# Performance work log

Hardware: AMD Instinct MI355X
Metric: run time of the kernel (lower is better)

The kernel has to match this reference:

```python
import jax, jax.numpy as jnp
import numpy as np

B, L = 8, 16384
H = 64          # num_channel
N2 = 32         # s4_hidden_size // 2 complex conjugate-pair modes
DEPTH = 4       # model_depth
NLAYERS = 1 + DEPTH  # number of DSSM layers
EPS = 1e-5


def setup_inputs() -> dict:
    key = jax.random.key(0)
    ks = jax.random.split(key, 12)
    x = jax.random.normal(ks[0], (B, L), dtype=jnp.float32)
    # input linear 1 -> H
    w_in = jax.random.normal(ks[1], (H,), dtype=jnp.float32)
    b_in = jax.random.normal(ks[2], (H,), dtype=jnp.float32) * 0.1
    # hidden linears H -> H
    w_mid = jax.random.normal(ks[3], (DEPTH, H, H), dtype=jnp.float32) / np.sqrt(H)
    b_mid = jax.random.normal(ks[4], (DEPTH, H), dtype=jnp.float32) * 0.1
    # output linear H -> 1
    w_out = jax.random.normal(ks[5], (H,), dtype=jnp.float32) / np.sqrt(H)
    b_out = jax.random.normal(ks[6], (), dtype=jnp.float32) * 0.1
    # S4D / DSSM parameters (stacked over the 5 SSM layers)
    log_dt = (jax.random.uniform(ks[7], (NLAYERS, H), dtype=jnp.float32)
              * (np.log(0.1) - np.log(0.001)) + np.log(0.001))
    log_A_real = jnp.log(0.5 * jnp.ones((NLAYERS, H, N2), dtype=jnp.float32))
    A_imag = jnp.pi * jnp.broadcast_to(jnp.arange(N2, dtype=jnp.float32), (NLAYERS, H, N2))
    C_re = jax.random.normal(ks[8], (NLAYERS, H, N2), dtype=jnp.float32)
    C_im = jax.random.normal(ks[9], (NLAYERS, H, N2), dtype=jnp.float32)
    D = jax.random.normal(ks[10], (NLAYERS, H), dtype=jnp.float32)
    return {"x": x, "w_in": w_in, "b_in": b_in, "w_mid": w_mid, "b_mid": b_mid,
            "w_out": w_out, "b_out": b_out, "log_dt": log_dt,
            "log_A_real": log_A_real, "A_imag": A_imag,
            "C_re": C_re, "C_im": C_im, "D": D}


def _dssm(u, log_dt, log_A_real, A_imag, C_re, C_im, D):
    # u: [B, H, L]; diagonal SSM applied as FFT convolution (S4D ZOH kernel)
    Lq = u.shape[-1]
    dt = jnp.exp(log_dt)                      # [H]
    A = -jnp.exp(log_A_real) + 1j * A_imag    # [H, N2]
    dtA = A * dt[:, None]                     # [H, N2]
    C_eff = (C_re + 1j * C_im) * (jnp.exp(dtA) - 1.0) / A
    # Vandermonde: exp(dtA * l) for l in [0, L)
    V = jnp.exp(dtA[:, :, None] * jnp.arange(Lq, dtype=jnp.float32))  # [H, N2, L]
    k = 2.0 * jnp.einsum('hn,hnl->hl', C_eff, V).real                # [H, L]
    uf = jnp.fft.rfft(u, n=2 * Lq)
    kf = jnp.fft.rfft(k, n=2 * Lq)
    y = jnp.fft.irfft(uf * kf, n=2 * Lq)[..., :Lq]
    return y + u * D[:, None]


def reference(x, w_in, b_in, w_mid, b_mid, w_out, b_out,
              log_dt, log_A_real, A_imag, C_re, C_im, D):
    # side chain: Abs -> Decibel -> Linear(1,H) -> tanh -> [DSSM -> tanh] ...
    s = 20.0 * jnp.log10(jnp.abs(x) + EPS)            # [B, L]
    h = jnp.tanh(s[..., None] * w_in + b_in)          # [B, L, H]
    h = jnp.tanh(_dssm(h.transpose(0, 2, 1), log_dt[0], log_A_real[0],
                       A_imag[0], C_re[0], C_im[0], D[0]).transpose(0, 2, 1))
    for i in range(DEPTH):
        h = jnp.tanh(jnp.einsum('blh,oh->blo', h, w_mid[i]) + b_mid[i])
        j = i + 1
        h = jnp.tanh(_dssm(h.transpose(0, 2, 1), log_dt[j], log_A_real[j],
                           A_imag[j], C_re[j], C_im[j], D[j]).transpose(0, 2, 1))
    g = jnp.einsum('blh,h->bl', h, w_out) + b_out      # [B, L]
    g = jnp.power(10.0, g / 20.0)                      # Amplitude (dB -> linear)
    return x * g
```

## Files before the change

### kernel.cpp

```cpp
#include <hip/hip_runtime.h>
#include <math.h>

#define Bq 8
#define Lq 16384
#define Hq 64
#define N2q 32
#define NLAYERSq 5

typedef _Float16 f16x8 __attribute__((ext_vector_type(8)));
typedef _Float16 f16x4 __attribute__((ext_vector_type(4)));
typedef _Float16 f16x2 __attribute__((ext_vector_type(2)));
typedef float    f32x4 __attribute__((ext_vector_type(4)));

#define MFMA16F(a, b, c) __builtin_amdgcn_mfma_f32_16x16x32_f16(a, b, c, 0, 0, 0)

#define UT_OFF    0
#define SS_OFF    32768
#define SMEM_SZ   50176
#define YST_OFF   0

#define WT_OFF_B   0
#define WP_OFF_B   163840
#define A2_OFF_B   (163840 + 5242880)
#define W16_OFF_B  (163840 + 5242880 + 15728640)
#define U_OFF_B    (163840 + 5242880 + 15728640 + 32768)

__device__ __forceinline__ float fast_tanh(float y) {
    float e = __expf(2.0f * y);
    return 1.0f - 2.0f * __builtin_amdgcn_rcpf(e + 1.0f);
}

__global__ __launch_bounds__(256)
void k_prep(const float* __restrict__ log_dt, const float* __restrict__ log_A_real,
            const float* __restrict__ A_imag, const float* __restrict__ C_re,
            const float* __restrict__ C_im, const float* __restrict__ Dvec,
            const float* __restrict__ w_mid,
            float* __restrict__ wT_tab, _Float16* __restrict__ Wp,
            _Float16* __restrict__ A2, _Float16* __restrict__ W16) {
    __shared__ float Pr[129][33], Pi[129][33];
    __shared__ float cre[32], cim[32], Kv[128];
    __shared__ double sdAr[32], sdAi[32];
    const int ph = blockIdx.x >> 2;
    const int qt = blockIdx.x & 3;
    const int tid = threadIdx.x;

    if (qt == 0 && ph < 256 && tid < 64) {
        int e = ph * 64 + tid;
        W16[e] = (_Float16)w_mid[e];
    }

    if (tid < 32) {
        int n = tid;
        int pidx = ph * N2q + n;
        double dt  = exp((double)log_dt[ph]);
        double aRe = -exp((double)log_A_real[pidx]);
        double aIm = (double)A_imag[pidx];
        double dAr = aRe * dt, dAi = aIm * dt;
        sdAr[n] = dAr; sdAi[n] = dAi;
        double er  = exp(dAr);
        double wre = er * cos(dAi), wim = er * sin(dAi);
        double Er = wre - 1.0, Ei = wim;
        double inv = 1.0 / (aRe * aRe + aIm * aIm);
        double Fr = (Er * aRe + Ei * aIm) * inv;
        double Fi = (Ei * aRe - Er * aIm) * inv;
        double Cr = (double)C_re[pidx], Ci = (double)C_im[pidx];
        cre[n] = (float)(2.0 * (Cr * Fr - Ci * Fi));
        cim[n] = (float)(2.0 * (Cr * Fi + Ci * Fr));
        if (qt == 0) {
            double qr = wre, qi = wim;
            #pragma unroll
            for (int s = 0; s < 7; s++) {
                double nr = qr * qr - qi * qi;
                qi = 2.0 * qr * qi; qr = nr;
            }
            float wTr = (float)qr, wTi = (float)qi;
            #pragma unroll
            for (int s = 0; s < 4; s++) {
                double nr = qr * qr - qi * qi;
                qi = 2.0 * qr * qi; qr = nr;
            }
            float* wt = wT_tab + ph * 128 + n * 4;
            wt[0] = wTr; wt[1] = wTi; wt[2] = (float)qr; wt[3] = (float)qi;
        }
    }
    __syncthreads();

    const double TWO_PI  = 6.2831853071795864769;
    const double INV_2PI = 0.15915494309189533577;
    for (int e = tid; e < 129 * 32; e += 256) {
        int j = e >> 5, n = e & 31;
        double phd = (double)j * sdAi[n];
        double r   = fma(-TWO_PI, nearbyint(phd * INV_2PI), phd);
        float  mag = __expf((float)((double)j * sdAr[n]));
        float  rf  = (float)r;
        Pr[j][n] = mag * cosf(rf);
        Pi[j][n] = mag * sinf(rf);
    }
    __syncthreads();

    if (tid < 128) {
        int d = tid;
        float s = 0.f;
        #pragma unroll 8
        for (int n = 0; n < 32; n++)
            s += cre[n] * Pr[d][n] - cim[n] * Pi[d][n];
        if (d == 0) s += Dvec[ph];
        Kv[d] = s;
    }
    __syncthreads();

    {
        _Float16* wpb = Wp + (size_t)ph * 8192;
        int o = tid;
        int kk = (qt << 4) + (o >> 4);
        int l0 = (o & 15) * 8;
        f16x8 v;
        #pragma unroll
        for (int j = 0; j < 8; j++) {
            int l = l0 + j;
            v[j] = (_Float16)((kk < 32) ? Pr[127 - l][kk] : Pi[127 - l][kk - 32]);
        }
        *(f16x8*)(wpb + kk * 128 + l0) = v;
    }
    {
        _Float16* a2b = A2 + (size_t)ph * 24576;
        for (int o = tid; o < 768; o += 256) {
            int m  = (qt << 5) + (o / 24);
            int k0 = (o % 24) * 8;
            f16x8 v;
            #pragma unroll
            for (int j = 0; j < 8; j++) {
                int k = k0 + j;
                float f;
                if (k < 128) {
                    f = (k <= m) ? Kv[m - k] : 0.f;
                } else {
                    int kk = k - 128, n2 = kk & 31;
                    float pr = Pr[m + 1][n2], pi2 = Pi[m + 1][n2];
                    f = (kk < 32) ? (cre[n2] * pr - cim[n2] * pi2)
                                  : -(cre[n2] * pi2 + cim[n2] * pr);
                }
                v[j] = (_Float16)f;
            }
            *(f16x8*)(a2b + m * 192 + k0) = v;
        }
    }
}

__global__ __launch_bounds__(256, 3)
void k_scan(const float* __restrict__ x, _Float16* __restrict__ u16,
            const _Float16* __restrict__ Wp_all, const _Float16* __restrict__ A2_all,
            const float* __restrict__ wT_all, int layer,
            const float* __restrict__ w_in, const float* __restrict__ b_in) {
    extern __shared__ char smem[];
    char* UT = smem + UT_OFF;
    char* Sf = smem + SS_OFF;
    char* St = smem + SS_OFF;
    char* yst = smem + YST_OFF;

    const int bh = blockIdx.x;
    const int h  = bh & 63;
    const int tid = threadIdx.x;
    const int lane = tid & 63;
    const int wave = tid >> 6;
    const int ph = layer * 64 + h;
    const _Float16* Wp = Wp_all + (size_t)ph * 8192;
    const _Float16* A2 = A2_all + (size_t)ph * 24576;
    const float* wT4 = wT_all + ph * 128;
    _Float16* uu = u16 + ((size_t)bh << 14);

    const int rA = lane & 15;
    const int qA = lane >> 4;

    if (layer == 0) {
        const float* xb = x + ((size_t)(bh >> 6) << 14);
        const float wi = w_in[h], bi = b_in[h];
        for (int it = 0; it < 8; ++it) {
            int flat8 = (it * 256 + tid) * 8;
            int n = flat8 >> 7, k = flat8 & 127;
            float4 a = *(const float4*)(xb + flat8);
            float4 b = *(const float4*)(xb + flat8 + 4);
            float f[8] = {a.x, a.y, a.z, a.w, b.x, b.y, b.z, b.w};
            f16x8 hv;
            #pragma unroll
            for (int j = 0; j < 8; j++) {
                float s = 6.0205999132796239f * __log2f(fabsf(f[j]) + 1e-5f);
                hv[j] = (_Float16)fast_tanh(fmaf(s, wi, bi));
            }
            *(f16x8*)(UT + n * 256 + ((k * 2) ^ ((n & 7) << 4))) = hv;
        }
    } else {
        for (int it = 0; it < 8; ++it) {
            int flat8 = (it * 256 + tid) * 8;
            int n = flat8 >> 7, k = flat8 & 127;
            f16x8 hv = *(const f16x8*)(uu + flat8);
            *(f16x8*)(UT + n * 256 + ((k * 2) ^ ((n & 7) << 4))) = hv;
        }
    }
    __syncthreads();

    {
        f32x4 acc1[8];
        #pragma unroll
        for (int nt = 0; nt < 8; nt++) acc1[nt] = (f32x4){0.f, 0.f, 0.f, 0.f};
        for (int ks = 0; ks < 4; ks++) {
            f16x8 af = *(const f16x8*)(Wp + (wave * 16 + rA) * 128 + ks * 32 + qA * 8);
            #pragma unroll
            for (int nt = 0; nt < 8; nt++) {
                int n = nt * 16 + rA;
                f16x8 bv = *(const f16x8*)(UT + n * 256 + ((ks * 64 + qA * 16) ^ ((n & 7) << 4)));
                acc1[nt] = MFMA16F(af, bv, acc1[nt]);
            }
        }
        #pragma unroll
        for (int nt = 0; nt < 8; nt++) {
            int c = nt * 16 + rA;
            #pragma unroll
            for (int r = 0; r < 4; r++)
                *(_Float16*)(Sf + (wave * 16 + qA * 4 + r) * 272 + c * 2) = (_Float16)acc1[nt][r];
        }
    }
    __syncthreads();

    {
        const int sn = tid >> 3;
        const int ss = tid & 7;
        const float wTr = wT4[sn * 4 + 0], wTi = wT4[sn * 4 + 1];
        float fr[16], fi[16];
        {
            f16x8 a0 = *(const f16x8*)(Sf + sn * 272 + ss * 32);
            f16x8 a1 = *(const f16x8*)(Sf + sn * 272 + ss * 32 + 16);
            f16x8 b0 = *(const f16x8*)(Sf + (sn + 32) * 272 + ss * 32);
            f16x8 b1 = *(const f16x8*)(Sf + (sn + 32) * 272 + ss * 32 + 16);
            #pragma unroll
            for (int j = 0; j < 8; j++) {
                fr[j] = (float)a0[j]; fr[j + 8] = (float)a1[j];
                fi[j] = (float)b0[j]; fi[j + 8] = (float)b1[j];
            }
        }
        float Tr = 0.f, Ti = 0.f;
        #pragma unroll
        for (int i = 0; i < 16; i++) {
            float nTr = fmaf(wTr, Tr, fmaf(-wTi, Ti, fr[i]));
            Ti = fmaf(wTr, Ti, fmaf(wTi, Tr, fi[i]));
            Tr = nTr;
        }
        float gr = wT4[sn * 4 + 2], gi = wT4[sn * 4 + 3];
        #pragma unroll
        for (int s = 0; s < 3; s++) {
            float pr = __shfl_up(Tr, 1 << s, 8);
            float pi = __shfl_up(Ti, 1 << s, 8);
            if (ss >= (1 << s)) {
                Tr = fmaf(gr, pr, fmaf(-gi, pi, Tr));
                Ti = fmaf(gr, pi, fmaf(gi, pr, Ti));
            }
            float ngr = fmaf(gr, gr, -gi * gi);
            gi = 2.f * gr * gi; gr = ngr;
        }
        float Er_ = __shfl_up(Tr, 1, 8);
        float Ei_ = __shfl_up(Ti, 1, 8);
        if (ss == 0) { Er_ = 0.f; Ei_ = 0.f; }
        __syncthreads();
        float Gr = Er_, Gi = Ei_;
        #pragma unroll
        for (int i = 0; i < 16; i++) {
            int c = ss * 16 + i;
            int sw = (c & 7) << 4;
            *(_Float16*)(St + c * 128 + ((sn * 2) ^ sw))        = (_Float16)Gr;
            *(_Float16*)(St + c * 128 + (((sn + 32) * 2) ^ sw)) = (_Float16)Gi;
            float nGr = fmaf(wTr, Gr, fmaf(-wTi, Gi, fr[i]));
            Gi = fmaf(wTr, Gi, fmaf(wTi, Gr, fi[i]));
            Gr = nGr;
        }
    }
    __syncthreads();

    f32x4 acc[2][8];
    #pragma unroll
    for (int mi = 0; mi < 2; mi++)
        #pragma unroll
        for (int nt = 0; nt < 8; nt++) acc[mi][nt] = (f32x4){0.f, 0.f, 0.f, 0.f};
    #pragma unroll
    for (int mi = 0; mi < 2; mi++) {
        const _Float16* Arow = A2 + ((wave * 2 + mi) * 16 + rA) * 192;
        for (int ks = 0; ks < 4; ks++) {
            f16x8 af = *(const f16x8*)(Arow + ks * 32 + qA * 8);
            #pragma unroll
            for (int nt = 0; nt < 8; nt++) {
                int n = nt * 16 + rA;
                f16x8 bv = *(const f16x8*)(UT + n * 256 + ((ks * 64 + qA * 16) ^ ((n & 7) << 4)));
                acc[mi][nt] = MFMA16F(af, bv, acc[mi][nt]);
            }
        }
        #pragma unroll
        for (int ks2 = 0; ks2 < 2; ks2++) {
            f16x8 af = *(const f16x8*)(Arow + 128 + ks2 * 32 + qA * 8);
            #pragma unroll
            for (int nt = 0; nt < 8; nt++) {
                int c = nt * 16 + rA;
                f16x8 bv = *(const f16x8*)(St + c * 128 + ((ks2 * 64 + qA * 16) ^ ((c & 7) << 4)));
                acc[mi][nt] = MFMA16F(af, bv, acc[mi][nt]);
            }
        }
    }
    __syncthreads();

    #pragma unroll
    for (int mi = 0; mi < 2; mi++) {
        int m0 = (wave * 2 + mi) * 16 + qA * 4;
        #pragma unroll
        for (int nt = 0; nt < 8; nt++) {
            int c = nt * 16 + rA;
            f16x4 o;
            o[0] = (_Float16)fast_tanh(acc[mi][nt][0]);
            o[1] = (_Float16)fast_tanh(acc[mi][nt][1]);
            o[2] = (_Float16)fast_tanh(acc[mi][nt][2]);
            o[3] = (_Float16)fast_tanh(acc[mi][nt][3]);
            *(f16x4*)(yst + c * 272 + m0 * 2) = o;
        }
    }
    __syncthreads();
    for (int it = 0; it < 8; ++it) {
        int e = it * 256 + tid;
        int c = e >> 4, l8 = e & 15;
        f16x8 hv = *(const f16x8*)(yst + c * 272 + l8 * 16);
        *(f16x8*)(uu + c * 128 + l8 * 8) = hv;
    }
}

__global__ __launch_bounds__(256, 4)
void k_linear(_Float16* __restrict__ uio, const _Float16* __restrict__ W16,
              const float* __restrict__ bias) {
    __shared__ __align__(16) char lmem[33792];
    _Float16* Ul  = (_Float16*)lmem;
    _Float16* yst = (_Float16*)lmem;

    const int b   = blockIdx.y;
    const int l0  = blockIdx.x * 256;
    const int tid = threadIdx.x;
    const int lane = tid & 63;
    const int wave = tid >> 6;
    const int rA = lane & 15;
    const int qA = lane >> 4;

    _Float16* ub = uio + ((size_t)b << 20) + l0;

    for (int it = 0; it < 4; ++it) {
        int g  = it * 256 + tid;
        int hp = g >> 5;
        int l8 = g & 31;
        f16x8 v0 = *(const f16x8*)(ub + (size_t)(hp * 2)     * Lq + l8 * 8);
        f16x8 v1 = *(const f16x8*)(ub + (size_t)(hp * 2 + 1) * Lq + l8 * 8);
        const unsigned short* p0 = (const unsigned short*)&v0;
        const unsigned short* p1 = (const unsigned short*)&v1;
        int sw = (l8 & 7) << 4;
        #pragma unroll
        for (int j = 0; j < 8; j++) {
            unsigned int pk = (unsigned int)p0[j] | ((unsigned int)p1[j] << 16);
            *(unsigned int*)((char*)Ul + (l8 * 8 + j) * 128 + ((hp * 4) ^ sw)) = pk;
        }
    }
    __syncthreads();

    f32x4 acc[16];
    #pragma unroll
    for (int nt = 0; nt < 16; nt++) acc[nt] = (f32x4){0.f, 0.f, 0.f, 0.f};
    const _Float16* Wrow = W16 + (wave * 16 + rA) * 64;
    #pragma unroll
    for (int kf = 0; kf < 2; kf++) {
        f16x8 af = *(const f16x8*)(Wrow + kf * 32 + qA * 8);
        #pragma unroll
        for (int nt = 0; nt < 16; nt++) {
            int n = nt * 16 + rA;
            int sw = ((n >> 3) & 7) << 4;
            f16x8 bv = *(const f16x8*)((char*)Ul + n * 128 + ((kf * 64 + qA * 16) ^ sw));
            acc[nt] = MFMA16F(af, bv, acc[nt]);
        }
    }
    __syncthreads();

    {
        int ob = wave * 16 + qA * 4;
        float bo0 = bias[ob], bo1 = bias[ob + 1], bo2 = bias[ob + 2], bo3 = bias[ob + 3];
        #pragma unroll
        for (int nt = 0; nt < 16; nt++) {
            int l = nt * 16 + rA;
            yst[(ob + 0) * 264 + l] = (_Float16)fast_tanh(acc[nt][0] + bo0);
            yst[(ob + 1) * 264 + l] = (_Float16)fast_tanh(acc[nt][1] + bo1);
            yst[(ob + 2) * 264 + l] = (_Float16)fast_tanh(acc[nt][2] + bo2);
            yst[(ob + 3) * 264 + l] = (_Float16)fast_tanh(acc[nt][3] + bo3);
        }
    }
    __syncthreads();
    for (int it = 0; it < 8; ++it) {
        int e = it * 256 + tid;
        int o = e >> 5, l8 = e & 31;
        f16x8 hv = *(const f16x8*)(yst + o * 264 + l8 * 8);
        *(f16x8*)(ub + (size_t)o * Lq + l8 * 8) = hv;
    }
}

__global__ __launch_bounds__(256)
void k_out(const _Float16* __restrict__ u16, const float* __restrict__ x,
           const float* __restrict__ w_out, const float* __restrict__ b_out,
           float* __restrict__ out) {
    int idx2 = (blockIdx.x * 256 + threadIdx.x) * 2;
    int b = idx2 >> 14;
    int l = idx2 & (Lq - 1);
    const _Float16* up = u16 + ((size_t)b << 20) + l;
    float acc0 = 0.f, acc1 = 0.f;
    #pragma unroll 8
    for (int hh = 0; hh < 64; ++hh) {
        f16x2 v = *(const f16x2*)(up + ((size_t)hh << 14));
        float w = w_out[hh];
        acc0 = fmaf(w, (float)v[0], acc0);
        acc1 = fmaf(w, (float)v[1], acc1);
    }
    float bo = b_out[0];
    float2 xv = *(const float2*)(x + idx2);
    float2 o;
    o.x = xv.x * exp2f((acc0 + bo) * 0.16609640474436812f);
    o.y = xv.y * exp2f((acc1 + bo) * 0.16609640474436812f);
    *(float2*)(out + idx2) = o;
}

extern "C" void kernel_launch(void* const* d_in, const int* in_sizes, int n_in,
                              void* d_out, int out_size, void* d_ws, size_t ws_size,
                              hipStream_t stream) {
    const float* x          = (const float*)d_in[0];
    const float* w_in       = (const float*)d_in[1];
    const float* b_in       = (const float*)d_in[2];
    const float* w_mid      = (const float*)d_in[3];
    const float* b_mid      = (const float*)d_in[4];
    const float* w_out      = (const float*)d_in[5];
    const float* b_out      = (const float*)d_in[6];
    const float* log_dt     = (const float*)d_in[7];
    const float* log_A_real = (const float*)d_in[8];
    const float* A_imag     = (const float*)d_in[9];
    const float* C_re       = (const float*)d_in[10];
    const float* C_im       = (const float*)d_in[11];
    const float* Dv         = (const float*)d_in[12];

    char* ws = (char*)d_ws;
    float*     wT_tab = (float*)(ws + WT_OFF_B);
    _Float16*  Wp     = (_Float16*)(ws + WP_OFF_B);
    _Float16*  A2     = (_Float16*)(ws + A2_OFF_B);
    _Float16*  W16    = (_Float16*)(ws + W16_OFF_B);
    _Float16*  u16    = (_Float16*)(ws + U_OFF_B);
    float* out = (float*)d_out;

    hipFuncSetAttribute((const void*)k_scan,
                        hipFuncAttributeMaxDynamicSharedMemorySize, SMEM_SZ);

    k_prep<<<NLAYERSq * Hq * 4, 256, 0, stream>>>(log_dt, log_A_real, A_imag,
                                                  C_re, C_im, Dv, w_mid,
                                                  wT_tab, Wp, A2, W16);
    for (int layer = 0; layer < NLAYERSq; layer++) {
        if (layer > 0)
            k_linear<<<dim3(Lq / 256, Bq), 256, 0, stream>>>(
                u16, W16 + (size_t)(layer - 1) * Hq * Hq, b_mid + (size_t)(layer - 1) * Hq);
        k_scan<<<Bq * Hq, 256, SMEM_SZ, stream>>>(x, u16, Wp, A2, wT_tab, layer,
                                                  w_in, b_in);
    }
    k_out<<<(Bq * Lq) / 512, 256, 0, stream>>>(u16, x, w_out, b_out, out);
}
```

Baseline: 176.3 us.

## Split each scan sequence across two blocks with flag-based carry handoff

Each (batch, channel) scan is split into two half-length blocks, giving 1024 blocks per layer instead of 512. The first half publishes its final state through global memory and a release flag. The second half spins on that flag and adds the carried-in state, scaled by powers of the decay factor, to its chunk states. Shared memory is shrunk so occupancy can rise to four blocks per CU. The spin-wait relies on first-half blocks being scheduled before or alongside second-half blocks, and it adds a flag-reset kernel.

```diff
diff --git a/kernel.cpp b/kernel.cpp
--- a/kernel.cpp
+++ b/kernel.cpp
@@ -15,19 +15,28 @@
 #define MFMA16F(a, b, c) __builtin_amdgcn_mfma_f32_16x16x32_f16(a, b, c, 0, 0, 0)
 
 #define UT_OFF    0
-#define SS_OFF    32768
-#define SMEM_SZ   50176
+#define SF_OFF    16384
+#define ST_OFF    25600
+#define SMEM_SZ   33792
 #define YST_OFF   0
 
 #define WT_OFF_B   0
 #define WP_OFF_B   163840
-#define A2_OFF_B   (163840 + 5242880)
-#define W16_OFF_B  (163840 + 5242880 + 15728640)
-#define U_OFF_B    (163840 + 5242880 + 15728640 + 32768)
+#define A2_OFF_B   5406720
+#define W16_OFF_B  21135360
+#define U_OFF_B    21168128
+#define FLAG_OFF_B 37945344
+#define T0_OFF_B   37955584
 
 __device__ __forceinline__ float fast_tanh(float y) {
     float e = __expf(2.0f * y);
     return 1.0f - 2.0f * __builtin_amdgcn_rcpf(e + 1.0f);
+}
+
+__global__ __launch_bounds__(256)
+void k_init(unsigned int* __restrict__ flags) {
+    int i = blockIdx.x * 256 + threadIdx.x;
+    if (i < NLAYERSq * 512) flags[i] = 0u;
 }
 
 __global__ __launch_bounds__(256)
@@ -75,7 +84,7 @@
             }
             float wTr = (float)qr, wTi = (float)qi;
             #pragma unroll
-            for (int s = 0; s < 4; s++) {
+            for (int s = 0; s < 3; s++) {
                 double nr = qr * qr - qi * qi;
                 qi = 2.0 * qr * qi; qr = nr;
             }
@@ -147,18 +156,20 @@
     }
 }
 
-__global__ __launch_bounds__(256, 3)
+__global__ __launch_bounds__(256, 4)
 void k_scan(const float* __restrict__ x, _Float16* __restrict__ u16,
             const _Float16* __restrict__ Wp_all, const _Float16* __restrict__ A2_all,
             const float* __restrict__ wT_all, int layer,
-            const float* __restrict__ w_in, const float* __restrict__ b_in) {
+            const float* __restrict__ w_in, const float* __restrict__ b_in,
+            unsigned int* __restrict__ flags, float* __restrict__ T0g) {
     extern __shared__ char smem[];
     char* UT = smem + UT_OFF;
-    char* Sf = smem + SS_OFF;
-    char* St = smem + SS_OFF;
+    char* Sf = smem + SF_OFF;
+    char* St = smem + ST_OFF;
     char* yst = smem + YST_OFF;
 
-    const int bh = blockIdx.x;
+    const int bh   = blockIdx.x & 511;
+    const int half = blockIdx.x >> 9;
     const int h  = bh & 63;
     const int tid = threadIdx.x;
     const int lane = tid & 63;
@@ -167,15 +178,17 @@
     const _Float16* Wp = Wp_all + (size_t)ph * 8192;
     const _Float16* A2 = A2_all + (size_t)ph * 24576;
     const float* wT4 = wT_all + ph * 128;
-    _Float16* uu = u16 + ((size_t)bh << 14);
+    _Float16* uu = u16 + ((size_t)bh << 14) + (half << 13);
+    unsigned int* flg = flags + layer * 512 + bh;
+    float* T0p = T0g + ((size_t)(layer * 512 + bh)) * 64;
 
     const int rA = lane & 15;
     const int qA = lane >> 4;
 
     if (layer == 0) {
-        const float* xb = x + ((size_t)(bh >> 6) << 14);
+        const float* xb = x + ((size_t)(bh >> 6) << 14) + (half << 13);
         const float wi = w_in[h], bi = b_in[h];
-        for (int it = 0; it < 8; ++it) {
+        for (int it = 0; it < 4; ++it) {
             int flat8 = (it * 256 + tid) * 8;
             int n = flat8 >> 7, k = flat8 & 127;
             float4 a = *(const float4*)(xb + flat8);
@@ -190,7 +203,7 @@
             *(f16x8*)(UT + n * 256 + ((k * 2) ^ ((n & 7) << 4))) = hv;
         }
     } else {
-        for (int it = 0; it < 8; ++it) {
+        for (int it = 0; it < 4; ++it) {
             int flat8 = (it * 256 + tid) * 8;
             int n = flat8 >> 7, k = flat8 & 127;
             f16x8 hv = *(const f16x8*)(uu + flat8);
@@ -200,24 +213,24 @@
     __syncthreads();
 
     {
-        f32x4 acc1[8];
-        #pragma unroll
-        for (int nt = 0; nt < 8; nt++) acc1[nt] = (f32x4){0.f, 0.f, 0.f, 0.f};
+        f32x4 acc1[4];
+        #pragma unroll
+        for (int nt = 0; nt < 4; nt++) acc1[nt] = (f32x4){0.f, 0.f, 0.f, 0.f};
         for (int ks = 0; ks < 4; ks++) {
             f16x8 af = *(const f16x8*)(Wp + (wave * 16 + rA) * 128 + ks * 32 + qA * 8);
             #pragma unroll
-            for (int nt = 0; nt < 8; nt++) {
+            for (int nt = 0; nt < 4; nt++) {
                 int n = nt * 16 + rA;
                 f16x8 bv = *(const f16x8*)(UT + n * 256 + ((ks * 64 + qA * 16) ^ ((n & 7) << 4)));
                 acc1[nt] = MFMA16F(af, bv, acc1[nt]);
             }
         }
         #pragma unroll
-        for (int nt = 0; nt < 8; nt++) {
+        for (int nt = 0; nt < 4; nt++) {
             int c = nt * 16 + rA;
             #pragma unroll
             for (int r = 0; r < 4; r++)
-                *(_Float16*)(Sf + (wave * 16 + qA * 4 + r) * 272 + c * 2) = (_Float16)acc1[nt][r];
+                *(_Float16*)(Sf + (wave * 16 + qA * 4 + r) * 144 + c * 2) = (_Float16)acc1[nt][r];
         }
     }
     __syncthreads();
@@ -226,21 +239,16 @@
         const int sn = tid >> 3;
         const int ss = tid & 7;
         const float wTr = wT4[sn * 4 + 0], wTi = wT4[sn * 4 + 1];
-        float fr[16], fi[16];
+        float fr[8], fi[8];
         {
-            f16x8 a0 = *(const f16x8*)(Sf + sn * 272 + ss * 32);
-            f16x8 a1 = *(const f16x8*)(Sf + sn * 272 + ss * 32 + 16);
-            f16x8 b0 = *(const f16x8*)(Sf + (sn + 32) * 272 + ss * 32);
-            f16x8 b1 = *(const f16x8*)(Sf + (sn + 32) * 272 + ss * 32 + 16);
-            #pragma unroll
-            for (int j = 0; j < 8; j++) {
-                fr[j] = (float)a0[j]; fr[j + 8] = (float)a1[j];
-                fi[j] = (float)b0[j]; fi[j + 8] = (float)b1[j];
-            }
+            f16x8 a0 = *(const f16x8*)(Sf + sn * 144 + ss * 16);
+            f16x8 b0 = *(const f16x8*)(Sf + (sn + 32) * 144 + ss * 16);
+            #pragma unroll
+            for (int j = 0; j < 8; j++) { fr[j] = (float)a0[j]; fi[j] = (float)b0[j]; }
         }
         float Tr = 0.f, Ti = 0.f;
         #pragma unroll
-        for (int i = 0; i < 16; i++) {
+        for (int i = 0; i < 8; i++) {
             float nTr = fmaf(wTr, Tr, fmaf(-wTi, Ti, fr[i]));
             Ti = fmaf(wTr, Ti, fmaf(wTi, Tr, fi[i]));
             Tr = nTr;
@@ -260,33 +268,77 @@
         float Er_ = __shfl_up(Tr, 1, 8);
         float Ei_ = __shfl_up(Ti, 1, 8);
         if (ss == 0) { Er_ = 0.f; Ei_ = 0.f; }
-        __syncthreads();
-        float Gr = Er_, Gi = Ei_;
-        #pragma unroll
-        for (int i = 0; i < 16; i++) {
-            int c = ss * 16 + i;
-            int sw = (c & 7) << 4;
-            *(_Float16*)(St + c * 128 + ((sn * 2) ^ sw))        = (_Float16)Gr;
-            *(_Float16*)(St + c * 128 + (((sn + 32) * 2) ^ sw)) = (_Float16)Gi;
-            float nGr = fmaf(wTr, Gr, fmaf(-wTi, Gi, fr[i]));
-            Gi = fmaf(wTr, Gi, fmaf(wTi, Gr, fi[i]));
-            Gr = nGr;
-        }
-    }
-    __syncthreads();
-
-    f32x4 acc[2][8];
+
+        if (half == 0) {
+            if (ss == 7) {
+                __hip_atomic_store(&T0p[sn * 2 + 0], Tr, __ATOMIC_RELEASE,
+                                   __HIP_MEMORY_SCOPE_AGENT);
+                __hip_atomic_store(&T0p[sn * 2 + 1], Ti, __ATOMIC_RELEASE,
+                                   __HIP_MEMORY_SCOPE_AGENT);
+            }
+            float Gr = Er_, Gi = Ei_;
+            #pragma unroll
+            for (int i = 0; i < 8; i++) {
+                int c = ss * 8 + i;
+                int sw = (c & 7) << 4;
+                *(_Float16*)(St + c * 128 + ((sn * 2) ^ sw))        = (_Float16)Gr;
+                *(_Float16*)(St + c * 128 + (((sn + 32) * 2) ^ sw)) = (_Float16)Gi;
+                float nGr = fmaf(wTr, Gr, fmaf(-wTi, Gi, fr[i]));
+                Gi = fmaf(wTr, Gi, fmaf(wTi, Gr, fi[i]));
+                Gr = nGr;
+            }
+            __syncthreads();
+            if (tid == 0)
+                __hip_atomic_store(flg, 1u, __ATOMIC_RELEASE,
+                                   __HIP_MEMORY_SCOPE_AGENT);
+        } else {
+            if (tid == 0) {
+                while (__hip_atomic_load(flg, __ATOMIC_ACQUIRE,
+                                         __HIP_MEMORY_SCOPE_AGENT) == 0u)
+                    __builtin_amdgcn_s_sleep(1);
+            }
+            __syncthreads();
+            float t0r = __hip_atomic_load(&T0p[sn * 2 + 0], __ATOMIC_RELAXED,
+                                          __HIP_MEMORY_SCOPE_AGENT);
+            float t0i = __hip_atomic_load(&T0p[sn * 2 + 1], __ATOMIC_RELAXED,
+                                          __HIP_MEMORY_SCOPE_AGENT);
+            float w8r = wT4[sn * 4 + 2], w8i = wT4[sn * 4 + 3];
+            float pwr = 1.f, pwi = 0.f;
+            for (int j = 0; j < ss; j++) {
+                float npr = pwr * w8r - pwi * w8i;
+                pwi = pwr * w8i + pwi * w8r; pwr = npr;
+            }
+            float Gr = Er_, Gi = Ei_;
+            #pragma unroll
+            for (int i = 0; i < 8; i++) {
+                int c = ss * 8 + i;
+                int sw = (c & 7) << 4;
+                float cr = Gr + (pwr * t0r - pwi * t0i);
+                float ci = Gi + (pwr * t0i + pwi * t0r);
+                *(_Float16*)(St + c * 128 + ((sn * 2) ^ sw))        = (_Float16)cr;
+                *(_Float16*)(St + c * 128 + (((sn + 32) * 2) ^ sw)) = (_Float16)ci;
+                float nGr = fmaf(wTr, Gr, fmaf(-wTi, Gi, fr[i]));
+                Gi = fmaf(wTr, Gi, fmaf(wTi, Gr, fi[i]));
+                Gr = nGr;
+                float npr = pwr * wTr - pwi * wTi;
+                pwi = pwr * wTi + pwi * wTr; pwr = npr;
+            }
+            __syncthreads();
+        }
+    }
+
+    f32x4 acc[2][4];
     #pragma unroll
     for (int mi = 0; mi < 2; mi++)
         #pragma unroll
-        for (int nt = 0; nt < 8; nt++) acc[mi][nt] = (f32x4){0.f, 0.f, 0.f, 0.f};
+        for (int nt = 0; nt < 4; nt++) acc[mi][nt] = (f32x4){0.f, 0.f, 0.f, 0.f};
     #pragma unroll
     for (int mi = 0; mi < 2; mi++) {
         const _Float16* Arow = A2 + ((wave * 2 + mi) * 16 + rA) * 192;
         for (int ks = 0; ks < 4; ks++) {
             f16x8 af = *(const f16x8*)(Arow + ks * 32 + qA * 8);
             #pragma unroll
-            for (int nt = 0; nt < 8; nt++) {
+            for (int nt = 0; nt < 4; nt++) {
                 int n = nt * 16 + rA;
                 f16x8 bv = *(const f16x8*)(UT + n * 256 + ((ks * 64 + qA * 16) ^ ((n & 7) << 4)));
                 acc[mi][nt] = MFMA16F(af, bv, acc[mi][nt]);
@@ -296,7 +348,7 @@
         for (int ks2 = 0; ks2 < 2; ks2++) {
             f16x8 af = *(const f16x8*)(Arow + 128 + ks2 * 32 + qA * 8);
             #pragma unroll
-            for (int nt = 0; nt < 8; nt++) {
+            for (int nt = 0; nt < 4; nt++) {
                 int c = nt * 16 + rA;
                 f16x8 bv = *(const f16x8*)(St + c * 128 + ((ks2 * 64 + qA * 16) ^ ((c & 7) << 4)));
                 acc[mi][nt] = MFMA16F(af, bv, acc[mi][nt]);
@@ -309,7 +361,7 @@
     for (int mi = 0; mi < 2; mi++) {
         int m0 = (wave * 2 + mi) * 16 + qA * 4;
         #pragma unroll
-        for (int nt = 0; nt < 8; nt++) {
+        for (int nt = 0; nt < 4; nt++) {
             int c = nt * 16 + rA;
             f16x4 o;
             o[0] = (_Float16)fast_tanh(acc[mi][nt][0]);
@@ -320,7 +372,7 @@
         }
     }
     __syncthreads();
-    for (int it = 0; it < 8; ++it) {
+    for (int it = 0; it < 4; ++it) {
         int e = it * 256 + tid;
         int c = e >> 4, l8 = e & 15;
         f16x8 hv = *(const f16x8*)(yst + c * 272 + l8 * 16);
@@ -442,16 +494,19 @@
     const float* Dv         = (const float*)d_in[12];
 
     char* ws = (char*)d_ws;
-    float*     wT_tab = (float*)(ws + WT_OFF_B);
-    _Float16*  Wp     = (_Float16*)(ws + WP_OFF_B);
-    _Float16*  A2     = (_Float16*)(ws + A2_OFF_B);
-    _Float16*  W16    = (_Float16*)(ws + W16_OFF_B);
-    _Float16*  u16    = (_Float16*)(ws + U_OFF_B);
+    float*        wT_tab = (float*)(ws + WT_OFF_B);
+    _Float16*     Wp     = (_Float16*)(ws + WP_OFF_B);
+    _Float16*     A2     = (_Float16*)(ws + A2_OFF_B);
+    _Float16*     W16    = (_Float16*)(ws + W16_OFF_B);
+    _Float16*     u16    = (_Float16*)(ws + U_OFF_B);
+    unsigned int* flags  = (unsigned int*)(ws + FLAG_OFF_B);
+    float*        T0g    = (float*)(ws + T0_OFF_B);
     float* out = (float*)d_out;
 
     hipFuncSetAttribute((const void*)k_scan,
                         hipFuncAttributeMaxDynamicSharedMemorySize, SMEM_SZ);
 
+    k_init<<<(NLAYERSq * 512 + 255) / 256, 256, 0, stream>>>(flags);
     k_prep<<<NLAYERSq * Hq * 4, 256, 0, stream>>>(log_dt, log_A_real, A_imag,
                                                   C_re, C_im, Dv, w_mid,
                                                   wT_tab, Wp, A2, W16);
@@ -459,8 +514,8 @@
         if (layer > 0)
             k_linear<<<dim3(Lq / 256, Bq), 256, 0, stream>>>(
                 u16, W16 + (size_t)(layer - 1) * Hq * Hq, b_mid + (size_t)(layer - 1) * Hq);
-        k_scan<<<Bq * Hq, 256, SMEM_SZ, stream>>>(x, u16, Wp, A2, wT_tab, layer,
-                                                  w_in, b_in);
+        k_scan<<<1024, 256, SMEM_SZ, stream>>>(x, u16, Wp, A2, wT_tab, layer,
+                                               w_in, b_in, flags, T0g);
     }
     k_out<<<(Bq * Lq) / 512, 256, 0, stream>>>(u16, x, w_out, b_out, out);
 }
```

After: 413.0 us. 134% more time.
